# Kernel optimization log

Hardware: AMD Instinct MI355X
Metric: run time of the kernel (lower is better)

The kernel has to match this reference:

```python
import jax, jax.numpy as jnp
import numpy as np

KS = 7       # neighborhood kernel size (fixed in __init__)
HEADS = 8    # num_heads (fixed in __init__)
LN_EPS = 1e-5


def _nbr_idx(L, k):
    # NATTEN-style clamped window: window start shifts inward at borders (no padding)
    starts = jnp.clip(jnp.arange(L) - k // 2, 0, L - k)
    idx = starts[:, None] + jnp.arange(k)            # [L, k] absolute neighbor coords
    rel = idx - jnp.arange(L)[:, None] + (k - 1)     # [L, k] rel-pos-bias index in [0, 2k-2]
    return idx, rel


def _na2d(x, qkv_w, qkv_b, proj_w, proj_b, rpb):
    # x: [B, H, W, C]  -> neighborhood attention with clamped 7x7 windows
    B, H, W, C = x.shape
    hd = C // HEADS
    qkv = x @ qkv_w.T + qkv_b                        # [B,H,W,3C]
    q, k, v = jnp.split(qkv, 3, axis=-1)
    q = q.reshape(B, H, W, HEADS, hd) * (hd ** -0.5)
    k = k.reshape(B, H, W, HEADS, hd)
    v = v.reshape(B, H, W, HEADS, hd)
    ri, rri = _nbr_idx(H, KS)                        # [H,KS]
    ci, rci = _nbr_idx(W, KS)                        # [W,KS]
    # gather neighborhoods: [B,H,W,KS,KS,heads,hd]
    kn = k[:, ri[:, None, :, None], ci[None, :, None, :]]
    vn = v[:, ri[:, None, :, None], ci[None, :, None, :]]
    scores = jnp.einsum('bijhd,bijpqhd->bhijpq', q, kn)   # [B,heads,H,W,KS,KS]
    bias = rpb[:, rri[:, None, :, None], rci[None, :, None, :]]  # [heads,H,W,KS,KS]
    scores = scores + bias[None]
    attn = jax.nn.softmax(scores.reshape(B, HEADS, H, W, KS * KS), axis=-1)
    vn = vn.reshape(B, H, W, KS * KS, HEADS, hd)
    out = jnp.einsum('bhijp,bijphd->bijhd', attn, vn)      # [B,H,W,heads,hd]
    out = out.reshape(B, H, W, C)
    return out @ proj_w.T + proj_b


def _layernorm(x, g, b):
    mu = jnp.mean(x, axis=-1, keepdims=True)
    var = jnp.mean((x - mu) ** 2, axis=-1, keepdims=True)
    return (x - mu) * jax.lax.rsqrt(var + LN_EPS) * g + b


def setup_inputs() -> dict:
    key = jax.random.key(0)
    ks = jax.random.split(key, 4)
    B, T, H, W, C = 2, 8, 48, 48, 64
    return {
        'q': jax.random.normal(ks[0], (B, T, H, W, C), dtype=jnp.float32),
        'qkv_w': jax.random.normal(ks[1], (3 * C, C), dtype=jnp.float32) * 0.02,
        'qkv_b': jnp.zeros((3 * C,), jnp.float32),
        'proj_w': jax.random.normal(ks[2], (C, C), dtype=jnp.float32) * 0.02,
        'proj_b': jnp.zeros((C,), jnp.float32),
        'rpb': jax.random.normal(ks[3], (HEADS, 2 * KS - 1, 2 * KS - 1), dtype=jnp.float32) * 0.02,
        'ln_g': jnp.ones((C,), jnp.float32),
        'ln_b': jnp.zeros((C,), jnp.float32),
    }


def reference(q, qkv_w, qkv_b, proj_w, proj_b, rpb, ln_g, ln_b):
    B, T, H, W, C = q.shape
    x = q.reshape(B * T, H, W, C)                    # '(b t) h w c'
    x = _na2d(x, qkv_w, qkv_b, proj_w, proj_b, rpb)  # wPT path
    x = x.reshape(B, T, H, W, C)
    return _layernorm(x, ln_g, ln_b)                 # norm_q; wGC=False
```

## Files before the change

kernel.cpp:

```cpp
#include <hip/hip_runtime.h>
#include <hip/hip_bf16.h>

#define IH   48
#define IW   48
#define CH   64
#define KS   7
#define LN_EPS 1e-5f
#define QSCALE 0.35355339059327373f
#define L2E    1.4426950408889634f

#define TSH  6
#define TSW  12
#define TPX  72
#define HSH  12
#define HSW  18
#define HP   216
#define KVS  136
#define AOS  72
#define RPBN 1352

typedef __bf16 bf16_t;
typedef bf16_t bf16x8 __attribute__((ext_vector_type(8)));
typedef float  f32x4  __attribute__((ext_vector_type(4)));
typedef float  f32x2  __attribute__((ext_vector_type(2)));

__device__ __forceinline__ float bflo(unsigned u) { union { unsigned i; float f; } v; v.i = u << 16; return v.f; }
__device__ __forceinline__ float bfhi(unsigned u) { union { unsigned i; float f; } v; v.i = u & 0xffff0000u; return v.f; }
__device__ __forceinline__ f32x2 unp2(unsigned u) { f32x2 r; r.x = bflo(u); r.y = bfhi(u); return r; }

__device__ __forceinline__ bf16x8 pack_bf16x8(float4 lo, float4 hi) {
    bf16x8 r;
    r[0] = (bf16_t)lo.x; r[1] = (bf16_t)lo.y; r[2] = (bf16_t)lo.z; r[3] = (bf16_t)lo.w;
    r[4] = (bf16_t)hi.x; r[5] = (bf16_t)hi.y; r[6] = (bf16_t)hi.z; r[7] = (bf16_t)hi.w;
    return r;
}

__global__ __launch_bounds__(576, 5) void fused_na_kernel(
        const float* __restrict__ x,
        const float* __restrict__ w,
        const float* __restrict__ b,
        const float* __restrict__ rpb,
        const float* __restrict__ pw,
        const float* __restrict__ pb,
        const float* __restrict__ g,
        const float* __restrict__ beta,
        float* __restrict__ out) {
    __shared__ __align__(16) __hip_bfloat16 kv[HP * KVS];
    __shared__ __align__(16) __hip_bfloat16 qao[TPX * AOS];
    __shared__ __align__(16) float rpbl[RPBN];

    const int blk  = blockIdx.x;
    const int n    = blk & 15;
    const int tile = blk >> 4;
    const int i0   = (tile >> 2) * TSH;
    const int j0   = (tile & 3) * TSW;
    int h0 = i0 - 3; h0 = h0 < 0 ? 0 : (h0 > IH - HSH ? IH - HSH : h0);
    int w0 = j0 - 3; w0 = w0 < 0 ? 0 : (w0 > IW - HSW ? IW - HSW : w0);
    const int tid = threadIdx.x;
    const size_t img = (size_t)n * (IH * IW);

    for (int idx = tid; idx < RPBN; idx += 576) rpbl[idx] = rpb[idx];

    {
        const int wv = tid >> 6;
        const int l  = tid & 63;
        const int m  = l & 15;
        const int kg = l >> 4;

        if (wv == 8) {
            const int ch_base = m * 4;
            const float4 bias4 = *(const float4*)(b + ch_base);
            bf16x8 wb0[4], wb1[4];
            #pragma unroll
            for (int t = 0; t < 4; ++t) {
                const float* wr_ = w + (size_t)(ch_base + t) * CH + kg * 8;
                wb0[t] = pack_bf16x8(*(const float4*)(wr_),      *(const float4*)(wr_ + 4));
                wb1[t] = pack_bf16x8(*(const float4*)(wr_ + 32), *(const float4*)(wr_ + 36));
            }
            for (int mt = 0; mt < 5; ++mt) {
                int px = mt * 16 + m; if (px > TPX - 1) px = TPX - 1;
                const int hr = i0 + px / TSW;
                const int wc = j0 + px % TSW;
                const float* xr = x + (img + hr * IW + wc) * CH + kg * 8;
                const bf16x8 a0 = pack_bf16x8(*(const float4*)(xr),      *(const float4*)(xr + 4));
                const bf16x8 a1 = pack_bf16x8(*(const float4*)(xr + 32), *(const float4*)(xr + 36));
                float val[4][4];
                #pragma unroll
                for (int t = 0; t < 4; ++t) {
                    f32x4 acc = {0.f, 0.f, 0.f, 0.f};
                    acc = __builtin_amdgcn_mfma_f32_16x16x32_bf16(a0, wb0[t], acc, 0, 0, 0);
                    acc = __builtin_amdgcn_mfma_f32_16x16x32_bf16(a1, wb1[t], acc, 0, 0, 0);
                    const float bias = (t == 0) ? bias4.x : (t == 1) ? bias4.y : (t == 2) ? bias4.z : bias4.w;
                    #pragma unroll
                    for (int rr = 0; rr < 4; ++rr) val[t][rr] = (acc[rr] + bias) * (QSCALE * L2E);
                }
                #pragma unroll
                for (int rr = 0; rr < 4; ++rr) {
                    const int pix = mt * 16 + kg * 4 + rr;
                    if (pix < TPX) {
                        union { ushort4 u; __hip_bfloat16 hh[4]; } pk;
                        #pragma unroll
                        for (int t = 0; t < 4; ++t) pk.hh[t] = __float2bfloat16(val[t][rr]);
                        *reinterpret_cast<ushort4*>(qao + pix * AOS + ch_base) = pk.u;
                    }
                }
            }
        } else {
            const int grp = 1 + (wv >> 2);
            const int wg  = wv & 3;
            const int ch_base = grp * 64 + m * 4;
            const float4 bias4 = *(const float4*)(b + ch_base);
            bf16x8 wb0[4], wb1[4];
            #pragma unroll
            for (int t = 0; t < 4; ++t) {
                const float* wr_ = w + (size_t)(ch_base + t) * CH + kg * 8;
                wb0[t] = pack_bf16x8(*(const float4*)(wr_),      *(const float4*)(wr_ + 4));
                wb1[t] = pack_bf16x8(*(const float4*)(wr_ + 32), *(const float4*)(wr_ + 36));
            }
            for (int mt = wg; mt < 14; mt += 4) {
                int hp = mt * 16 + m; if (hp > HP - 1) hp = HP - 1;
                const int hr = h0 + hp / HSW;
                const int wc = w0 + hp % HSW;
                const float* xr = x + (img + hr * IW + wc) * CH + kg * 8;
                const bf16x8 a0 = pack_bf16x8(*(const float4*)(xr),      *(const float4*)(xr + 4));
                const bf16x8 a1 = pack_bf16x8(*(const float4*)(xr + 32), *(const float4*)(xr + 36));
                float val[4][4];
                #pragma unroll
                for (int t = 0; t < 4; ++t) {
                    f32x4 acc = {0.f, 0.f, 0.f, 0.f};
                    acc = __builtin_amdgcn_mfma_f32_16x16x32_bf16(a0, wb0[t], acc, 0, 0, 0);
                    acc = __builtin_amdgcn_mfma_f32_16x16x32_bf16(a1, wb1[t], acc, 0, 0, 0);
                    const float bias = (t == 0) ? bias4.x : (t == 1) ? bias4.y : (t == 2) ? bias4.z : bias4.w;
                    #pragma unroll
                    for (int rr = 0; rr < 4; ++rr) val[t][rr] = acc[rr] + bias;
                }
                #pragma unroll
                for (int rr = 0; rr < 4; ++rr) {
                    const int pix = mt * 16 + kg * 4 + rr;
                    if (pix < HP) {
                        union { ushort4 u; __hip_bfloat16 hh[4]; } pk;
                        #pragma unroll
                        for (int t = 0; t < 4; ++t) pk.hh[t] = __float2bfloat16(val[t][rr]);
                        *reinterpret_cast<ushort4*>(kv + pix * KVS + (grp - 1) * 64 + m * 4) = pk.u;
                    }
                }
            }
        }
    }
    __syncthreads();

    {
        const int h  = tid & 7;
        const int px = tid >> 3;
        const int i  = i0 + px / TSW;
        const int j  = j0 + px % TSW;

        f32x2 q0[4];
        {
            const uint4 u = *reinterpret_cast<const uint4*>(qao + px * AOS + h * 8);
            q0[0] = unp2(u.x); q0[1] = unp2(u.y); q0[2] = unp2(u.z); q0[3] = unp2(u.w);
        }
        __syncthreads();

        int si = i - 3;  si = si < 0 ? 0 : (si > IH - KS ? IH - KS : si);
        int sj = j - 3;  sj = sj < 0 ? 0 : (sj > IW - KS ? IW - KS : sj);
        const float* rpc = rpbl + h * (2*KS-1) * (2*KS-1)
                                + (si - i + (KS-1)) * (2*KS-1) + (sj - j + (KS-1));
        const __hip_bfloat16* kbase = kv + ((si - h0) * HSW + (sj - w0)) * KVS + h * 8;

        float lr = 0.f;
        f32x2 a[4];
        #pragma unroll
        for (int d = 0; d < 4; ++d) a[d] = (f32x2){0.f, 0.f};

        for (int p = 0; p < KS; ++p) {
            const __hip_bfloat16* row = kbase + p * (HSW * KVS);
            uint4 kb[KS], vb[KS];
            #pragma unroll
            for (int qq = 0; qq < KS; ++qq) {
                kb[qq] = *reinterpret_cast<const uint4*>(row + qq * KVS);
                vb[qq] = *reinterpret_cast<const uint4*>(row + qq * KVS + 64);
            }
            float bl[KS];
            #pragma unroll
            for (int qq = 0; qq < KS; ++qq) bl[qq] = rpc[p * (2*KS-1) + qq];

            float s[KS];
            #pragma unroll
            for (int qq = 0; qq < KS; ++qq) {
                const f32x2 k0 = unp2(kb[qq].x), k1 = unp2(kb[qq].y);
                const f32x2 k2 = unp2(kb[qq].z), k3 = unp2(kb[qq].w);
                f32x2 t = q0[0]*k0 + q0[1]*k1 + q0[2]*k2 + q0[3]*k3;
                s[qq] = t.x + t.y;
            }
            float e[KS];
            #pragma unroll
            for (int qq = 0; qq < KS; ++qq)
                e[qq] = __builtin_amdgcn_exp2f(fmaf(bl[qq], L2E, s[qq]));

            #pragma unroll
            for (int qq = 0; qq < KS; ++qq) {
                const f32x2 v0 = unp2(vb[qq].x), v1 = unp2(vb[qq].y);
                const f32x2 v2 = unp2(vb[qq].z), v3 = unp2(vb[qq].w);
                lr += e[qq];
                a[0] += e[qq] * v0; a[1] += e[qq] * v1;
                a[2] += e[qq] * v2; a[3] += e[qq] * v3;
            }
        }
        const float inv = 1.f / lr;
        union { uint4 u; __hip_bfloat16 hh[8]; } pk;
        #pragma unroll
        for (int d = 0; d < 4; ++d) {
            pk.hh[2*d]   = __float2bfloat16(a[d].x * inv);
            pk.hh[2*d+1] = __float2bfloat16(a[d].y * inv);
        }
        *reinterpret_cast<uint4*>(qao + px * AOS + h * 8) = pk.u;
    }
    __syncthreads();

    if ((tid >> 6) < 5) {
        const int wv = tid >> 6;
        const int l  = tid & 63;
        const int m  = l & 15;
        const int kg = l >> 4;

        int ap = wv * 16 + m; if (ap > TPX - 1) ap = TPX - 1;
        const __hip_bfloat16* ar = qao + ap * AOS + kg * 8;
        const bf16x8 a0 = *reinterpret_cast<const bf16x8*>(ar);
        const bf16x8 a1 = *reinterpret_cast<const bf16x8*>(ar + 32);

        const int ch_base = m * 4;
        const float4 bias4 = *(const float4*)(pb + ch_base);

        float val[4][4];
        #pragma unroll
        for (int t = 0; t < 4; ++t) {
            const float* wr_ = pw + (size_t)(ch_base + t) * CH + kg * 8;
            const bf16x8 b0 = pack_bf16x8(*(const float4*)(wr_),      *(const float4*)(wr_ + 4));
            const bf16x8 b1 = pack_bf16x8(*(const float4*)(wr_ + 32), *(const float4*)(wr_ + 36));
            f32x4 acc = {0.f, 0.f, 0.f, 0.f};
            acc = __builtin_amdgcn_mfma_f32_16x16x32_bf16(a0, b0, acc, 0, 0, 0);
            acc = __builtin_amdgcn_mfma_f32_16x16x32_bf16(a1, b1, acc, 0, 0, 0);
            const float bias = (t == 0) ? bias4.x : (t == 1) ? bias4.y : (t == 2) ? bias4.z : bias4.w;
            #pragma unroll
            for (int r = 0; r < 4; ++r) val[t][r] = acc[r] + bias;
        }

        float sm[4];
        #pragma unroll
        for (int r = 0; r < 4; ++r) sm[r] = val[0][r] + val[1][r] + val[2][r] + val[3][r];
        #pragma unroll
        for (int mask = 1; mask <= 8; mask <<= 1) {
            #pragma unroll
            for (int r = 0; r < 4; ++r) sm[r] += __shfl_xor(sm[r], mask, 64);
        }
        float mu[4];
        #pragma unroll
        for (int r = 0; r < 4; ++r) mu[r] = sm[r] * (1.f / 64.f);

        float qs[4];
        #pragma unroll
        for (int r = 0; r < 4; ++r) {
            float aa = val[0][r] - mu[r], bq = val[1][r] - mu[r];
            float c  = val[2][r] - mu[r], d  = val[3][r] - mu[r];
            qs[r] = aa * aa + bq * bq + c * c + d * d;
        }
        #pragma unroll
        for (int mask = 1; mask <= 8; mask <<= 1) {
            #pragma unroll
            for (int r = 0; r < 4; ++r) qs[r] += __shfl_xor(qs[r], mask, 64);
        }
        float rs[4];
        #pragma unroll
        for (int r = 0; r < 4; ++r) rs[r] = rsqrtf(qs[r] * (1.f / 64.f) + LN_EPS);

        const float4 g4  = *(const float4*)(g + ch_base);
        const float4 be4 = *(const float4*)(beta + ch_base);
        #pragma unroll
        for (int r = 0; r < 4; ++r) {
            const int pl = wv * 16 + kg * 4 + r;
            if (pl < TPX) {
                const int gi = i0 + pl / TSW, gj = j0 + pl % TSW;
                float4 o;
                o.x = (val[0][r] - mu[r]) * rs[r] * g4.x + be4.x;
                o.y = (val[1][r] - mu[r]) * rs[r] * g4.y + be4.y;
                o.z = (val[2][r] - mu[r]) * rs[r] * g4.z + be4.z;
                o.w = (val[3][r] - mu[r]) * rs[r] * g4.w + be4.w;
                *reinterpret_cast<float4*>(out + (img + gi * IW + gj) * CH + ch_base) = o;
            }
        }
    }
}

extern "C" void kernel_launch(void* const* d_in, const int* in_sizes, int n_in,
                              void* d_out, int out_size, void* d_ws, size_t ws_size,
                              hipStream_t stream) {
    const float* x      = (const float*)d_in[0];
    const float* qkv_w  = (const float*)d_in[1];
    const float* qkv_b  = (const float*)d_in[2];
    const float* proj_w = (const float*)d_in[3];
    const float* proj_b = (const float*)d_in[4];
    const float* rpb    = (const float*)d_in[5];
    const float* ln_g   = (const float*)d_in[6];
    const float* ln_b   = (const float*)d_in[7];
    float* out = (float*)d_out;

    fused_na_kernel<<<512, 576, 0, stream>>>(x, qkv_w, qkv_b, rpb,
                                             proj_w, proj_b, ln_g, ln_b, out);
}
```

Measured before the change: 115.6 us.

## Shrink tiles to 6x8, split neighbor columns across thread pairs, rebalance QKV work

Tiles shrink from 6x12 to 6x8 pixels, so the grid grows from 512 to 768 blocks of 768 threads. The attention stage now uses two threads per (pixel, head), each covering alternating window columns, and combines their partial sums with a lane shuffle. The QKV projection work is unified into one strided loop over 25 MFMA tasks per block. The goal is more parallelism and shorter per-thread serial attention loops, at the cost of more halo recomputation of K/V (168 halo pixels per 48-pixel tile) and extra shuffles.

```diff
diff --git a/kernel.cpp b/kernel.cpp
--- a/kernel.cpp
+++ b/kernel.cpp
@@ -10,11 +10,11 @@
 #define L2E    1.4426950408889634f
 
 #define TSH  6
-#define TSW  12
-#define TPX  72
+#define TSW  8
+#define TPX  48
 #define HSH  12
-#define HSW  18
-#define HP   216
+#define HSW  14
+#define HP   168
 #define KVS  136
 #define AOS  72
 #define RPBN 1352
@@ -35,7 +35,7 @@
     return r;
 }
 
-__global__ __launch_bounds__(576, 5) void fused_na_kernel(
+__global__ __launch_bounds__(768, 3) void fused_na_kernel(
         const float* __restrict__ x,
         const float* __restrict__ w,
         const float* __restrict__ b,
@@ -52,14 +52,14 @@
     const int blk  = blockIdx.x;
     const int n    = blk & 15;
     const int tile = blk >> 4;
-    const int i0   = (tile >> 2) * TSH;
-    const int j0   = (tile & 3) * TSW;
+    const int i0   = (tile / 6) * TSH;
+    const int j0   = (tile % 6) * TSW;
     int h0 = i0 - 3; h0 = h0 < 0 ? 0 : (h0 > IH - HSH ? IH - HSH : h0);
     int w0 = j0 - 3; w0 = w0 < 0 ? 0 : (w0 > IW - HSW ? IW - HSW : w0);
     const int tid = threadIdx.x;
     const size_t img = (size_t)n * (IH * IW);
 
-    for (int idx = tid; idx < RPBN; idx += 576) rpbl[idx] = rpb[idx];
+    for (int idx = tid; idx < RPBN; idx += 768) rpbl[idx] = rpb[idx];
 
     {
         const int wv = tid >> 6;
@@ -67,9 +67,15 @@
         const int m  = l & 15;
         const int kg = l >> 4;
 
-        if (wv == 8) {
-            const int ch_base = m * 4;
+        for (int u = wv; u < 25; u += 12) {
+            int grp, mt;
+            if (u < 11)      { grp = 1; mt = u; }
+            else if (u < 22) { grp = 2; mt = u - 11; }
+            else             { grp = 0; mt = u - 22; }
+
+            const int ch_base = grp * 64 + m * 4;
             const float4 bias4 = *(const float4*)(b + ch_base);
+            const float scale = (grp == 0) ? (QSCALE * L2E) : 1.f;
             bf16x8 wb0[4], wb1[4];
             #pragma unroll
             for (int t = 0; t < 4; ++t) {
@@ -77,72 +83,39 @@
                 wb0[t] = pack_bf16x8(*(const float4*)(wr_),      *(const float4*)(wr_ + 4));
                 wb1[t] = pack_bf16x8(*(const float4*)(wr_ + 32), *(const float4*)(wr_ + 36));
             }
-            for (int mt = 0; mt < 5; ++mt) {
-                int px = mt * 16 + m; if (px > TPX - 1) px = TPX - 1;
-                const int hr = i0 + px / TSW;
-                const int wc = j0 + px % TSW;
-                const float* xr = x + (img + hr * IW + wc) * CH + kg * 8;
-                const bf16x8 a0 = pack_bf16x8(*(const float4*)(xr),      *(const float4*)(xr + 4));
-                const bf16x8 a1 = pack_bf16x8(*(const float4*)(xr + 32), *(const float4*)(xr + 36));
-                float val[4][4];
+
+            int hr, wc;
+            if (grp == 0) {
+                const int px = mt * 16 + m;
+                hr = i0 + (px >> 3); wc = j0 + (px & 7);
+            } else {
+                int hp = mt * 16 + m; if (hp > HP - 1) hp = HP - 1;
+                hr = h0 + hp / HSW;  wc = w0 + hp % HSW;
+            }
+            const float* xr = x + (img + hr * IW + wc) * CH + kg * 8;
+            const bf16x8 a0 = pack_bf16x8(*(const float4*)(xr),      *(const float4*)(xr + 4));
+            const bf16x8 a1 = pack_bf16x8(*(const float4*)(xr + 32), *(const float4*)(xr + 36));
+
+            float val[4][4];
+            #pragma unroll
+            for (int t = 0; t < 4; ++t) {
+                f32x4 acc = {0.f, 0.f, 0.f, 0.f};
+                acc = __builtin_amdgcn_mfma_f32_16x16x32_bf16(a0, wb0[t], acc, 0, 0, 0);
+                acc = __builtin_amdgcn_mfma_f32_16x16x32_bf16(a1, wb1[t], acc, 0, 0, 0);
+                const float bias = (t == 0) ? bias4.x : (t == 1) ? bias4.y : (t == 2) ? bias4.z : bias4.w;
                 #pragma unroll
-                for (int t = 0; t < 4; ++t) {
-                    f32x4 acc = {0.f, 0.f, 0.f, 0.f};
-                    acc = __builtin_amdgcn_mfma_f32_16x16x32_bf16(a0, wb0[t], acc, 0, 0, 0);
-                    acc = __builtin_amdgcn_mfma_f32_16x16x32_bf16(a1, wb1[t], acc, 0, 0, 0);
-                    const float bias = (t == 0) ? bias4.x : (t == 1) ? bias4.y : (t == 2) ? bias4.z : bias4.w;
-                    #pragma unroll
-                    for (int rr = 0; rr < 4; ++rr) val[t][rr] = (acc[rr] + bias) * (QSCALE * L2E);
-                }
+                for (int rr = 0; rr < 4; ++rr) val[t][rr] = (acc[rr] + bias) * scale;
+            }
+            #pragma unroll
+            for (int rr = 0; rr < 4; ++rr) {
+                const int pix = mt * 16 + kg * 4 + rr;
+                union { ushort4 u; __hip_bfloat16 hh[4]; } pk;
                 #pragma unroll
-                for (int rr = 0; rr < 4; ++rr) {
-                    const int pix = mt * 16 + kg * 4 + rr;
-                    if (pix < TPX) {
-                        union { ushort4 u; __hip_bfloat16 hh[4]; } pk;
-                        #pragma unroll
-                        for (int t = 0; t < 4; ++t) pk.hh[t] = __float2bfloat16(val[t][rr]);
-                        *reinterpret_cast<ushort4*>(qao + pix * AOS + ch_base) = pk.u;
-                    }
-                }
-            }
-        } else {
-            const int grp = 1 + (wv >> 2);
-            const int wg  = wv & 3;
-            const int ch_base = grp * 64 + m * 4;
-            const float4 bias4 = *(const float4*)(b + ch_base);
-            bf16x8 wb0[4], wb1[4];
-            #pragma unroll
-            for (int t = 0; t < 4; ++t) {
-                const float* wr_ = w + (size_t)(ch_base + t) * CH + kg * 8;
-                wb0[t] = pack_bf16x8(*(const float4*)(wr_),      *(const float4*)(wr_ + 4));
-                wb1[t] = pack_bf16x8(*(const float4*)(wr_ + 32), *(const float4*)(wr_ + 36));
-            }
-            for (int mt = wg; mt < 14; mt += 4) {
-                int hp = mt * 16 + m; if (hp > HP - 1) hp = HP - 1;
-                const int hr = h0 + hp / HSW;
-                const int wc = w0 + hp % HSW;
-                const float* xr = x + (img + hr * IW + wc) * CH + kg * 8;
-                const bf16x8 a0 = pack_bf16x8(*(const float4*)(xr),      *(const float4*)(xr + 4));
-                const bf16x8 a1 = pack_bf16x8(*(const float4*)(xr + 32), *(const float4*)(xr + 36));
-                float val[4][4];
-                #pragma unroll
-                for (int t = 0; t < 4; ++t) {
-                    f32x4 acc = {0.f, 0.f, 0.f, 0.f};
-                    acc = __builtin_amdgcn_mfma_f32_16x16x32_bf16(a0, wb0[t], acc, 0, 0, 0);
-                    acc = __builtin_amdgcn_mfma_f32_16x16x32_bf16(a1, wb1[t], acc, 0, 0, 0);
-                    const float bias = (t == 0) ? bias4.x : (t == 1) ? bias4.y : (t == 2) ? bias4.z : bias4.w;
-                    #pragma unroll
-                    for (int rr = 0; rr < 4; ++rr) val[t][rr] = acc[rr] + bias;
-                }
-                #pragma unroll
-                for (int rr = 0; rr < 4; ++rr) {
-                    const int pix = mt * 16 + kg * 4 + rr;
-                    if (pix < HP) {
-                        union { ushort4 u; __hip_bfloat16 hh[4]; } pk;
-                        #pragma unroll
-                        for (int t = 0; t < 4; ++t) pk.hh[t] = __float2bfloat16(val[t][rr]);
-                        *reinterpret_cast<ushort4*>(kv + pix * KVS + (grp - 1) * 64 + m * 4) = pk.u;
-                    }
+                for (int t = 0; t < 4; ++t) pk.hh[t] = __float2bfloat16(val[t][rr]);
+                if (grp == 0) {
+                    *reinterpret_cast<ushort4*>(qao + pix * AOS + m * 4) = pk.u;
+                } else if (pix < HP) {
+                    *reinterpret_cast<ushort4*>(kv + pix * KVS + (grp - 1) * 64 + m * 4) = pk.u;
                 }
             }
         }
@@ -150,10 +123,11 @@
     __syncthreads();
 
     {
-        const int h  = tid & 7;
-        const int px = tid >> 3;
-        const int i  = i0 + px / TSW;
-        const int j  = j0 + px % TSW;
+        const int half = tid & 1;
+        const int h    = (tid >> 1) & 7;
+        const int px   = tid >> 4;
+        const int i    = i0 + (px >> 3);
+        const int j    = j0 + (px & 7);
 
         f32x2 q0[4];
         {
@@ -164,68 +138,59 @@
 
         int si = i - 3;  si = si < 0 ? 0 : (si > IH - KS ? IH - KS : si);
         int sj = j - 3;  sj = sj < 0 ? 0 : (sj > IW - KS ? IW - KS : sj);
-        const float* rpc = rpbl + h * (2*KS-1) * (2*KS-1)
-                                + (si - i + (KS-1)) * (2*KS-1) + (sj - j + (KS-1));
-        const __hip_bfloat16* kbase = kv + ((si - h0) * HSW + (sj - w0)) * KVS + h * 8;
+        const float* rpc2 = rpbl + h * (2*KS-1) * (2*KS-1)
+                                 + (si - i + (KS-1)) * (2*KS-1) + (sj - j + (KS-1)) + half;
+        const __hip_bfloat16* kvb = kv + ((si - h0) * HSW + (sj - w0) + half) * KVS + h * 8;
 
         float lr = 0.f;
         f32x2 a[4];
         #pragma unroll
         for (int d = 0; d < 4; ++d) a[d] = (f32x2){0.f, 0.f};
 
+        #pragma unroll
         for (int p = 0; p < KS; ++p) {
-            const __hip_bfloat16* row = kbase + p * (HSW * KVS);
-            uint4 kb[KS], vb[KS];
-            #pragma unroll
-            for (int qq = 0; qq < KS; ++qq) {
-                kb[qq] = *reinterpret_cast<const uint4*>(row + qq * KVS);
-                vb[qq] = *reinterpret_cast<const uint4*>(row + qq * KVS + 64);
-            }
-            float bl[KS];
-            #pragma unroll
-            for (int qq = 0; qq < KS; ++qq) bl[qq] = rpc[p * (2*KS-1) + qq];
-
-            float s[KS];
-            #pragma unroll
-            for (int qq = 0; qq < KS; ++qq) {
-                const f32x2 k0 = unp2(kb[qq].x), k1 = unp2(kb[qq].y);
-                const f32x2 k2 = unp2(kb[qq].z), k3 = unp2(kb[qq].w);
-                f32x2 t = q0[0]*k0 + q0[1]*k1 + q0[2]*k2 + q0[3]*k3;
-                s[qq] = t.x + t.y;
-            }
-            float e[KS];
-            #pragma unroll
-            for (int qq = 0; qq < KS; ++qq)
-                e[qq] = __builtin_amdgcn_exp2f(fmaf(bl[qq], L2E, s[qq]));
-
-            #pragma unroll
-            for (int qq = 0; qq < KS; ++qq) {
-                const f32x2 v0 = unp2(vb[qq].x), v1 = unp2(vb[qq].y);
-                const f32x2 v2 = unp2(vb[qq].z), v3 = unp2(vb[qq].w);
-                lr += e[qq];
-                a[0] += e[qq] * v0; a[1] += e[qq] * v1;
-                a[2] += e[qq] * v2; a[3] += e[qq] * v3;
-            }
-        }
+            #pragma unroll
+            for (int cc = 0; cc < 4; ++cc) {
+                if (cc == 3 && half) continue;
+                const uint4 kb = *reinterpret_cast<const uint4*>(kvb + (p * HSW + 2 * cc) * KVS);
+                const uint4 vb = *reinterpret_cast<const uint4*>(kvb + (p * HSW + 2 * cc) * KVS + 64);
+                const float bl = rpc2[p * (2*KS-1) + 2 * cc];
+
+                f32x2 t = q0[0]*unp2(kb.x) + q0[1]*unp2(kb.y)
+                        + q0[2]*unp2(kb.z) + q0[3]*unp2(kb.w);
+                const float e = __builtin_amdgcn_exp2f(fmaf(bl, L2E, t.x + t.y));
+                lr += e;
+                a[0] += e * unp2(vb.x); a[1] += e * unp2(vb.y);
+                a[2] += e * unp2(vb.z); a[3] += e * unp2(vb.w);
+            }
+        }
+
+        #pragma unroll
+        for (int d = 0; d < 4; ++d) {
+            a[d].x += __shfl_xor(a[d].x, 1, 64);
+            a[d].y += __shfl_xor(a[d].y, 1, 64);
+        }
+        lr += __shfl_xor(lr, 1, 64);
         const float inv = 1.f / lr;
-        union { uint4 u; __hip_bfloat16 hh[8]; } pk;
-        #pragma unroll
-        for (int d = 0; d < 4; ++d) {
-            pk.hh[2*d]   = __float2bfloat16(a[d].x * inv);
-            pk.hh[2*d+1] = __float2bfloat16(a[d].y * inv);
-        }
-        *reinterpret_cast<uint4*>(qao + px * AOS + h * 8) = pk.u;
+
+        const f32x2 alo = half ? a[2] : a[0];
+        const f32x2 ahi = half ? a[3] : a[1];
+        union { uint2 u; __hip_bfloat16 hh[4]; } pk;
+        pk.hh[0] = __float2bfloat16(alo.x * inv);
+        pk.hh[1] = __float2bfloat16(alo.y * inv);
+        pk.hh[2] = __float2bfloat16(ahi.x * inv);
+        pk.hh[3] = __float2bfloat16(ahi.y * inv);
+        *reinterpret_cast<uint2*>(qao + px * AOS + h * 8 + half * 4) = pk.u;
     }
     __syncthreads();
 
-    if ((tid >> 6) < 5) {
+    if ((tid >> 6) < 3) {
         const int wv = tid >> 6;
         const int l  = tid & 63;
         const int m  = l & 15;
         const int kg = l >> 4;
 
-        int ap = wv * 16 + m; if (ap > TPX - 1) ap = TPX - 1;
-        const __hip_bfloat16* ar = qao + ap * AOS + kg * 8;
+        const __hip_bfloat16* ar = qao + (wv * 16 + m) * AOS + kg * 8;
         const bf16x8 a0 = *reinterpret_cast<const bf16x8*>(ar);
         const bf16x8 a1 = *reinterpret_cast<const bf16x8*>(ar + 32);
 
@@ -279,15 +244,13 @@
         #pragma unroll
         for (int r = 0; r < 4; ++r) {
             const int pl = wv * 16 + kg * 4 + r;
-            if (pl < TPX) {
-                const int gi = i0 + pl / TSW, gj = j0 + pl % TSW;
-                float4 o;
-                o.x = (val[0][r] - mu[r]) * rs[r] * g4.x + be4.x;
-                o.y = (val[1][r] - mu[r]) * rs[r] * g4.y + be4.y;
-                o.z = (val[2][r] - mu[r]) * rs[r] * g4.z + be4.z;
-                o.w = (val[3][r] - mu[r]) * rs[r] * g4.w + be4.w;
-                *reinterpret_cast<float4*>(out + (img + gi * IW + gj) * CH + ch_base) = o;
-            }
+            const int gi = i0 + (pl >> 3), gj = j0 + (pl & 7);
+            float4 o;
+            o.x = (val[0][r] - mu[r]) * rs[r] * g4.x + be4.x;
+            o.y = (val[1][r] - mu[r]) * rs[r] * g4.y + be4.y;
+            o.z = (val[2][r] - mu[r]) * rs[r] * g4.z + be4.z;
+            o.w = (val[3][r] - mu[r]) * rs[r] * g4.w + be4.w;
+            *reinterpret_cast<float4*>(out + (img + gi * IW + gj) * CH + ch_base) = o;
         }
     }
 }
@@ -305,6 +268,6 @@
     const float* ln_b   = (const float*)d_in[7];
     float* out = (float*)d_out;
 
-    fused_na_kernel<<<512, 576, 0, stream>>>(x, qkv_w, qkv_b, rpb,
+    fused_na_kernel<<<768, 768, 0, stream>>>(x, qkv_w, qkv_b, rpb,
                                              proj_w, proj_b, ln_g, ln_b, out);
 }
```

Result: slower. 139.7 us (+20.8%).

## Enlarge spatial tile to 12x12 and fuse K/V projection per wave

Applied to the files above, without the earlier changes.

Each block now covers a 12x12 output tile with an 18x18 halo instead of 6x12 with a 12x18 halo. This cuts the redundant K/V projection over overlapping halos and halves the grid to 256 blocks. The QKV stage is reorganised so each wave computes both K and V for a 16-pixel slab, with the Q tiles handled as extra work units. The attention loop runs twice per thread, and one barrier is dropped. The trade-off is a much larger LDS footprint and fewer, heavier blocks, which reduces occupancy and latency hiding.

```diff
diff --git a/kernel.cpp b/kernel.cpp
--- a/kernel.cpp
+++ b/kernel.cpp
@@ -9,12 +9,12 @@
 #define QSCALE 0.35355339059327373f
 #define L2E    1.4426950408889634f
 
-#define TSH  6
+#define TSH  12
 #define TSW  12
-#define TPX  72
-#define HSH  12
+#define TPX  144
+#define HSH  18
 #define HSW  18
-#define HP   216
+#define HP   324
 #define KVS  136
 #define AOS  72
 #define RPBN 1352
@@ -35,7 +35,7 @@
     return r;
 }
 
-__global__ __launch_bounds__(576, 5) void fused_na_kernel(
+__global__ __launch_bounds__(576, 2) void fused_na_kernel(
         const float* __restrict__ x,
         const float* __restrict__ w,
         const float* __restrict__ b,
@@ -67,91 +67,97 @@
         const int m  = l & 15;
         const int kg = l >> 4;
 
-        if (wv == 8) {
-            const int ch_base = m * 4;
-            const float4 bias4 = *(const float4*)(b + ch_base);
-            bf16x8 wb0[4], wb1[4];
-            #pragma unroll
-            for (int t = 0; t < 4; ++t) {
-                const float* wr_ = w + (size_t)(ch_base + t) * CH + kg * 8;
-                wb0[t] = pack_bf16x8(*(const float4*)(wr_),      *(const float4*)(wr_ + 4));
-                wb1[t] = pack_bf16x8(*(const float4*)(wr_ + 32), *(const float4*)(wr_ + 36));
-            }
-            for (int mt = 0; mt < 5; ++mt) {
-                int px = mt * 16 + m; if (px > TPX - 1) px = TPX - 1;
-                const int hr = i0 + px / TSW;
-                const int wc = j0 + px % TSW;
-                const float* xr = x + (img + hr * IW + wc) * CH + kg * 8;
-                const bf16x8 a0 = pack_bf16x8(*(const float4*)(xr),      *(const float4*)(xr + 4));
-                const bf16x8 a1 = pack_bf16x8(*(const float4*)(xr + 32), *(const float4*)(xr + 36));
-                float val[4][4];
-                #pragma unroll
-                for (int t = 0; t < 4; ++t) {
-                    f32x4 acc = {0.f, 0.f, 0.f, 0.f};
-                    acc = __builtin_amdgcn_mfma_f32_16x16x32_bf16(a0, wb0[t], acc, 0, 0, 0);
-                    acc = __builtin_amdgcn_mfma_f32_16x16x32_bf16(a1, wb1[t], acc, 0, 0, 0);
-                    const float bias = (t == 0) ? bias4.x : (t == 1) ? bias4.y : (t == 2) ? bias4.z : bias4.w;
-                    #pragma unroll
-                    for (int rr = 0; rr < 4; ++rr) val[t][rr] = (acc[rr] + bias) * (QSCALE * L2E);
-                }
-                #pragma unroll
-                for (int rr = 0; rr < 4; ++rr) {
-                    const int pix = mt * 16 + kg * 4 + rr;
-                    if (pix < TPX) {
-                        union { ushort4 u; __hip_bfloat16 hh[4]; } pk;
-                        #pragma unroll
-                        for (int t = 0; t < 4; ++t) pk.hh[t] = __float2bfloat16(val[t][rr]);
-                        *reinterpret_cast<ushort4*>(qao + pix * AOS + ch_base) = pk.u;
-                    }
-                }
-            }
-        } else {
-            const int grp = 1 + (wv >> 2);
-            const int wg  = wv & 3;
-            const int ch_base = grp * 64 + m * 4;
-            const float4 bias4 = *(const float4*)(b + ch_base);
-            bf16x8 wb0[4], wb1[4];
-            #pragma unroll
-            for (int t = 0; t < 4; ++t) {
-                const float* wr_ = w + (size_t)(ch_base + t) * CH + kg * 8;
-                wb0[t] = pack_bf16x8(*(const float4*)(wr_),      *(const float4*)(wr_ + 4));
-                wb1[t] = pack_bf16x8(*(const float4*)(wr_ + 32), *(const float4*)(wr_ + 36));
-            }
-            for (int mt = wg; mt < 14; mt += 4) {
-                int hp = mt * 16 + m; if (hp > HP - 1) hp = HP - 1;
+        bf16x8 wk0[4], wk1[4], wv0[4], wv1[4];
+        #pragma unroll
+        for (int t = 0; t < 4; ++t) {
+            const float* wrk = w + (size_t)(64 + m * 4 + t) * CH + kg * 8;
+            wk0[t] = pack_bf16x8(*(const float4*)(wrk),      *(const float4*)(wrk + 4));
+            wk1[t] = pack_bf16x8(*(const float4*)(wrk + 32), *(const float4*)(wrk + 36));
+            const float* wrv = w + (size_t)(128 + m * 4 + t) * CH + kg * 8;
+            wv0[t] = pack_bf16x8(*(const float4*)(wrv),      *(const float4*)(wrv + 4));
+            wv1[t] = pack_bf16x8(*(const float4*)(wrv + 32), *(const float4*)(wrv + 36));
+        }
+        const float4 biasK = *(const float4*)(b + 64 + m * 4);
+        const float4 biasV = *(const float4*)(b + 128 + m * 4);
+
+        for (int u = wv; u < 30; u += 9) {
+            if (u < 21) {
+                int hp = u * 16 + m; if (hp > HP - 1) hp = HP - 1;
                 const int hr = h0 + hp / HSW;
                 const int wc = w0 + hp % HSW;
                 const float* xr = x + (img + hr * IW + wc) * CH + kg * 8;
                 const bf16x8 a0 = pack_bf16x8(*(const float4*)(xr),      *(const float4*)(xr + 4));
                 const bf16x8 a1 = pack_bf16x8(*(const float4*)(xr + 32), *(const float4*)(xr + 36));
+
+                float valK[4][4], valV[4][4];
+                #pragma unroll
+                for (int t = 0; t < 4; ++t) {
+                    f32x4 ak = {0.f, 0.f, 0.f, 0.f};
+                    ak = __builtin_amdgcn_mfma_f32_16x16x32_bf16(a0, wk0[t], ak, 0, 0, 0);
+                    ak = __builtin_amdgcn_mfma_f32_16x16x32_bf16(a1, wk1[t], ak, 0, 0, 0);
+                    f32x4 av = {0.f, 0.f, 0.f, 0.f};
+                    av = __builtin_amdgcn_mfma_f32_16x16x32_bf16(a0, wv0[t], av, 0, 0, 0);
+                    av = __builtin_amdgcn_mfma_f32_16x16x32_bf16(a1, wv1[t], av, 0, 0, 0);
+                    const float bk = (t == 0) ? biasK.x : (t == 1) ? biasK.y : (t == 2) ? biasK.z : biasK.w;
+                    const float bv = (t == 0) ? biasV.x : (t == 1) ? biasV.y : (t == 2) ? biasV.z : biasV.w;
+                    #pragma unroll
+                    for (int rr = 0; rr < 4; ++rr) { valK[t][rr] = ak[rr] + bk; valV[t][rr] = av[rr] + bv; }
+                }
+                #pragma unroll
+                for (int rr = 0; rr < 4; ++rr) {
+                    const int pix = u * 16 + kg * 4 + rr;
+                    if (pix < HP) {
+                        union { ushort4 u4; __hip_bfloat16 hh[4]; } pk;
+                        #pragma unroll
+                        for (int t = 0; t < 4; ++t) pk.hh[t] = __float2bfloat16(valK[t][rr]);
+                        *reinterpret_cast<ushort4*>(kv + pix * KVS + m * 4) = pk.u4;
+                        #pragma unroll
+                        for (int t = 0; t < 4; ++t) pk.hh[t] = __float2bfloat16(valV[t][rr]);
+                        *reinterpret_cast<ushort4*>(kv + pix * KVS + 64 + m * 4) = pk.u4;
+                    }
+                }
+            } else {
+                const int mt = u - 21;
+                const int px = mt * 16 + m;
+                const int hr = i0 + px / TSW;
+                const int wc = j0 + px % TSW;
+                bf16x8 wq0[4], wq1[4];
+                #pragma unroll
+                for (int t = 0; t < 4; ++t) {
+                    const float* wr_ = w + (size_t)(m * 4 + t) * CH + kg * 8;
+                    wq0[t] = pack_bf16x8(*(const float4*)(wr_),      *(const float4*)(wr_ + 4));
+                    wq1[t] = pack_bf16x8(*(const float4*)(wr_ + 32), *(const float4*)(wr_ + 36));
+                }
+                const float4 biasQ = *(const float4*)(b + m * 4);
+                const float* xr = x + (img + hr * IW + wc) * CH + kg * 8;
+                const bf16x8 a0 = pack_bf16x8(*(const float4*)(xr),      *(const float4*)(xr + 4));
+                const bf16x8 a1 = pack_bf16x8(*(const float4*)(xr + 32), *(const float4*)(xr + 36));
                 float val[4][4];
                 #pragma unroll
                 for (int t = 0; t < 4; ++t) {
                     f32x4 acc = {0.f, 0.f, 0.f, 0.f};
-                    acc = __builtin_amdgcn_mfma_f32_16x16x32_bf16(a0, wb0[t], acc, 0, 0, 0);
-                    acc = __builtin_amdgcn_mfma_f32_16x16x32_bf16(a1, wb1[t], acc, 0, 0, 0);
-                    const float bias = (t == 0) ? bias4.x : (t == 1) ? bias4.y : (t == 2) ? bias4.z : bias4.w;
+                    acc = __builtin_amdgcn_mfma_f32_16x16x32_bf16(a0, wq0[t], acc, 0, 0, 0);
+                    acc = __builtin_amdgcn_mfma_f32_16x16x32_bf16(a1, wq1[t], acc, 0, 0, 0);
+                    const float bias = (t == 0) ? biasQ.x : (t == 1) ? biasQ.y : (t == 2) ? biasQ.z : biasQ.w;
                     #pragma unroll
-                    for (int rr = 0; rr < 4; ++rr) val[t][rr] = acc[rr] + bias;
+                    for (int rr = 0; rr < 4; ++rr) val[t][rr] = (acc[rr] + bias) * (QSCALE * L2E);
                 }
                 #pragma unroll
                 for (int rr = 0; rr < 4; ++rr) {
                     const int pix = mt * 16 + kg * 4 + rr;
-                    if (pix < HP) {
-                        union { ushort4 u; __hip_bfloat16 hh[4]; } pk;
-                        #pragma unroll
-                        for (int t = 0; t < 4; ++t) pk.hh[t] = __float2bfloat16(val[t][rr]);
-                        *reinterpret_cast<ushort4*>(kv + pix * KVS + (grp - 1) * 64 + m * 4) = pk.u;
-                    }
+                    union { ushort4 u4; __hip_bfloat16 hh[4]; } pk;
+                    #pragma unroll
+                    for (int t = 0; t < 4; ++t) pk.hh[t] = __float2bfloat16(val[t][rr]);
+                    *reinterpret_cast<ushort4*>(qao + pix * AOS + m * 4) = pk.u4;
                 }
             }
         }
     }
     __syncthreads();
 
-    {
+    for (int rep = 0; rep < 2; ++rep) {
         const int h  = tid & 7;
-        const int px = tid >> 3;
+        const int px = (tid >> 3) + rep * 72;
         const int i  = i0 + px / TSW;
         const int j  = j0 + px % TSW;
 
@@ -160,7 +166,6 @@
             const uint4 u = *reinterpret_cast<const uint4*>(qao + px * AOS + h * 8);
             q0[0] = unp2(u.x); q0[1] = unp2(u.y); q0[2] = unp2(u.z); q0[3] = unp2(u.w);
         }
-        __syncthreads();
 
         int si = i - 3;  si = si < 0 ? 0 : (si > IH - KS ? IH - KS : si);
         int sj = j - 3;  sj = sj < 0 ? 0 : (sj > IW - KS ? IW - KS : sj);
@@ -218,14 +223,13 @@
     }
     __syncthreads();
 
-    if ((tid >> 6) < 5) {
+    {
         const int wv = tid >> 6;
         const int l  = tid & 63;
         const int m  = l & 15;
         const int kg = l >> 4;
 
-        int ap = wv * 16 + m; if (ap > TPX - 1) ap = TPX - 1;
-        const __hip_bfloat16* ar = qao + ap * AOS + kg * 8;
+        const __hip_bfloat16* ar = qao + (wv * 16 + m) * AOS + kg * 8;
         const bf16x8 a0 = *reinterpret_cast<const bf16x8*>(ar);
         const bf16x8 a1 = *reinterpret_cast<const bf16x8*>(ar + 32);
 
@@ -279,15 +283,13 @@
         #pragma unroll
         for (int r = 0; r < 4; ++r) {
             const int pl = wv * 16 + kg * 4 + r;
-            if (pl < TPX) {
-                const int gi = i0 + pl / TSW, gj = j0 + pl % TSW;
-                float4 o;
-                o.x = (val[0][r] - mu[r]) * rs[r] * g4.x + be4.x;
-                o.y = (val[1][r] - mu[r]) * rs[r] * g4.y + be4.y;
-                o.z = (val[2][r] - mu[r]) * rs[r] * g4.z + be4.z;
-                o.w = (val[3][r] - mu[r]) * rs[r] * g4.w + be4.w;
-                *reinterpret_cast<float4*>(out + (img + gi * IW + gj) * CH + ch_base) = o;
-            }
+            const int gi = i0 + pl / TSW, gj = j0 + pl % TSW;
+            float4 o;
+            o.x = (val[0][r] - mu[r]) * rs[r] * g4.x + be4.x;
+            o.y = (val[1][r] - mu[r]) * rs[r] * g4.y + be4.y;
+            o.z = (val[2][r] - mu[r]) * rs[r] * g4.z + be4.z;
+            o.w = (val[3][r] - mu[r]) * rs[r] * g4.w + be4.w;
+            *reinterpret_cast<float4*>(out + (img + gi * IW + gj) * CH + ch_base) = o;
         }
     }
 }
@@ -305,6 +307,6 @@
     const float* ln_b   = (const float*)d_in[7];
     float* out = (float*)d_out;
 
-    fused_na_kernel<<<512, 576, 0, stream>>>(x, qkv_w, qkv_b, rpb,
+    fused_na_kernel<<<256, 576, 0, stream>>>(x, qkv_w, qkv_b, rpb,
                                              proj_w, proj_b, ln_g, ln_b, out);
 }
```

Result: faster. 112.2 us (-2.9%).
